# Kernel optimization log

Measured on AMD Instinct MI355X. Metric: run time of the kernel, lower is better.

## Reference

```python
import jax, jax.numpy as jnp
import numpy as np

B, H, N, D = 2, 8, 2048, 64


def setup_inputs() -> dict:
    key = jax.random.key(0)
    kq, kk, kv = jax.random.split(key, 3)
    q = jax.random.normal(kq, (B, H, N, D), dtype=jnp.float32)
    k = jax.random.normal(kk, (B, H, N, D), dtype=jnp.float32)
    v = jax.random.normal(kv, (B, H, N, D), dtype=jnp.float32)
    return {"q": q, "k": k, "v": v}


def _selective_attn(sim):
    # sim: (b, h, i, j). Gate computed from first head, relu'd, SOS unmasked,
    # diagonal zeroed, shifted down one row, cumsum over query rows, subtracted.
    b, h, i, j = sim.shape
    gate = jax.nn.relu(sim[:, 0])                       # (b, i, j)
    gate = gate.at[:, :, j - i].set(0.0)                # no_mask_sos: column -i
    eye = jnp.eye(i, dtype=sim.dtype)
    if j > i:
        eye = jnp.pad(eye, ((0, 0), (j - i, 0)), constant_values=1.0)
    gate = (1.0 - eye) * gate
    # F.pad(gate, (0,0,1,-1)): shift rows down by one, drop last row
    gate = jnp.pad(gate, ((0, 0), (1, 0), (0, 0)))[:, :i, :]
    gate = jnp.cumsum(gate, axis=-2)
    return sim - gate[:, None]                          # broadcast over heads


def reference(q, k, v):
    scale = q.shape[-1] ** -0.5
    i, j = q.shape[-2], k.shape[-2]

    # squared L2 distance scores: ||q||^2 + ||k||^2 - 2 q.k  (== cdist(q,k)**2)
    q_sq = jnp.sum(q * q, axis=-1)                      # (b, h, i)
    k_sq = jnp.sum(k * k, axis=-1)                      # (b, h, j)
    qk = jnp.einsum('bhid,bhjd->bhij', q, k)            # (b, h, i, j)
    d2 = jnp.maximum(q_sq[..., :, None] + k_sq[..., None, :] - 2.0 * qk, 0.0)
    sim = -d2 * scale

    # causal mask (triu with offset j - i + 1)
    mask_value = -jnp.finfo(sim.dtype).max
    causal = jnp.triu(jnp.ones((i, j), dtype=bool), j - i + 1)
    sim = jnp.where(causal, mask_value, sim)

    # selective attention gating
    sim = _selective_attn(sim)

    # one-hot straight-through attention
    idx = jnp.argmax(sim, axis=-1)                      # (b, h, i)
    hard = jax.nn.one_hot(idx, j, dtype=sim.dtype)      # (b, h, i, j)
    soft = jax.nn.softmax(sim, axis=-1)
    attn = hard + soft - jax.lax.stop_gradient(soft)

    return jnp.einsum('bhij,bhjd->bhid', attn, v)
```

## Files before the change

kernel.cpp:

```cpp
#include <hip/hip_runtime.h>
#include <stdint.h>

#define B_ 2
#define H_ 8
#define N_ 2048
#define D_ 64
#define BH_ (B_ * H_)
#define NROWS (BH_ * N_)
#define TPB_ 288
#define NTASK (TPB_ * BH_)
#define NBLK1 (NTASK / 4)
#define MAXCH 8
#define EPSF 8e-3f
#define INFF __int_as_float(0x7f800000)

using u64 = unsigned long long;
using u32 = unsigned int;
typedef __attribute__((ext_vector_type(8))) short short8;
typedef __attribute__((ext_vector_type(4))) float f32x4;

__global__ __launch_bounds__(256) void prep_k(
    const float* __restrict__ k, char* __restrict__ khi_g,
    char* __restrict__ klo_g, float* __restrict__ ksq_g,
    u32* __restrict__ count)
{
  if (blockIdx.x == 0 && threadIdx.x == 0) count[0] = 0;
  const int t = (int)blockIdx.x * 256 + threadIdx.x;
  const int r = t >> 3, kg = t & 7;
  const float* kp = k + (size_t)r * D_ + kg * 8;
  const float4 f0 = *(const float4*)kp;
  const float4 f1 = *(const float4*)(kp + 4);
  const float vv[8] = {f0.x, f0.y, f0.z, f0.w, f1.x, f1.y, f1.z, f1.w};
  u32 hw[4], lw[4];
  float ps = 0.f;
  #pragma unroll
  for (int e = 0; e < 4; ++e) {
    const float va = vv[2 * e], vb = vv[2 * e + 1];
    ps = fmaf(va, va, ps); ps = fmaf(vb, vb, ps);
    const u32 ha = __float_as_uint(va) & 0xFFFF0000u;
    const u32 hb = __float_as_uint(vb) & 0xFFFF0000u;
    hw[e] = (ha >> 16) | hb;
    const u32 la = __float_as_uint(va - __uint_as_float(ha));
    const u32 lb = __float_as_uint(vb - __uint_as_float(hb));
    lw[e] = (la >> 16) | (lb & 0xFFFF0000u);
  }
  const size_t off = ((size_t)(r >> 4) * 2 + (kg >> 2)) * 1024 +
                     (size_t)(((kg & 3) << 4) + (r & 15)) * 16;
  *(uint4*)(khi_g + off) = make_uint4(hw[0], hw[1], hw[2], hw[3]);
  *(uint4*)(klo_g + off) = make_uint4(lw[0], lw[1], lw[2], lw[3]);
  float ssum = ps;
  ssum += __shfl_xor(ssum, 1);
  ssum += __shfl_xor(ssum, 2);
  ssum += __shfl_xor(ssum, 4);
  if (kg == 0) ksq_g[r] = ssum;
}

__global__ __launch_bounds__(256, 4) void phase1(
    const float* __restrict__ q, const char* __restrict__ khi_g,
    const char* __restrict__ klo_g, const float* __restrict__ ksq_g,
    u64* __restrict__ bestc, u32* __restrict__ secc)
{
  const int b = (int)blockIdx.x;
  const int ob = (b & 7) * (NBLK1 / 8) + (b >> 3);
  const int task = ob * 4 + (threadIdx.x >> 6);
  const int bh = task / TPB_;
  int rem = task - bh * TPB_;
  int g2 = 0, nc = 1;
  while (rem >= nc) { rem -= nc; ++g2; nc = (2 * g2 + 17) >> 4; }
  const int c = rem;
  const int jfirst = c * 16;
  const int jlast = min(jfirst + 15, 2 * g2 + 1);

  const int lane = threadIdx.x & 63;
  const int grp = lane >> 4, c0 = lane & 15;
  const int i0 = g2 * 32;

  short8 ah[2][2], al[2][2];
  #pragma unroll
  for (int s = 0; s < 2; ++s) {
    const float* qrow =
        q + ((size_t)bh * N_ + i0 + s * 16 + c0) * D_ + grp * 8;
    #pragma unroll
    for (int h = 0; h < 2; ++h) {
      const float4 f0 = *(const float4*)(qrow + h * 32);
      const float4 f1 = *(const float4*)(qrow + h * 32 + 4);
      const float vv[8] = {f0.x, f0.y, f0.z, f0.w, f1.x, f1.y, f1.z, f1.w};
      #pragma unroll
      for (int e = 0; e < 8; ++e) {
        const float v = vv[e];
        const u32 hb = __float_as_uint(v) & 0xFFFF0000u;
        ah[s][h][e] = (short)(hb >> 16);
        al[s][h][e] = (short)(__float_as_uint(v - __uint_as_float(hb)) >> 16);
      }
    }
  }

  float bf[2][4], sf[2][4];
  u32 bj[2][4];
  #pragma unroll
  for (int s = 0; s < 2; ++s)
    #pragma unroll
    for (int r2 = 0; r2 < 4; ++r2) {
      bf[s][r2] = INFF; sf[s][r2] = INFF; bj[s][r2] = 0;
    }

  const size_t fb = (size_t)bh * 128 * 2048;
  const char* ph = khi_g + fb + (size_t)jfirst * 2048 + lane * 16;
  const char* pl = klo_g + fb + (size_t)jfirst * 2048 + lane * 16;
  const float* pk = ksq_g + (size_t)bh * N_ + jfirst * 16 + c0;

  short8 ch0 = *(const short8*)(ph);
  short8 ch1 = *(const short8*)(ph + 1024);
  short8 cl0 = *(const short8*)(pl);
  short8 cl1 = *(const short8*)(pl + 1024);
  float cks = *pk;

  for (int js = jfirst; js <= jlast; ++js) {
    const int adv = (js < jlast) ? 1 : 0;
    const char* nh = ph + adv * 2048;
    const char* nl = pl + adv * 2048;
    const short8 nh0 = *(const short8*)(nh);
    const short8 nh1 = *(const short8*)(nh + 1024);
    const short8 nl0 = *(const short8*)(nl);
    const short8 nl1 = *(const short8*)(nl + 1024);
    const float nks = pk[adv * 16];
    ph = nh; pl = nl; pk += adv * 16;

    const int jcol = js * 16 + c0;
    #pragma unroll
    for (int s = 0; s < 2; ++s) {
      if (js > 2 * g2 + s) continue;
      const bool dsub = (js == 2 * g2 + s);
      f32x4 aA = {0.f, 0.f, 0.f, 0.f}, aB = {0.f, 0.f, 0.f, 0.f};
      aA = __builtin_amdgcn_mfma_f32_16x16x32_bf16(ah[s][0], ch0, aA, 0, 0, 0);
      aB = __builtin_amdgcn_mfma_f32_16x16x32_bf16(ah[s][1], ch1, aB, 0, 0, 0);
      aA = __builtin_amdgcn_mfma_f32_16x16x32_bf16(ah[s][0], cl0, aA, 0, 0, 0);
      aB = __builtin_amdgcn_mfma_f32_16x16x32_bf16(ah[s][1], cl1, aB, 0, 0, 0);
      aA = __builtin_amdgcn_mfma_f32_16x16x32_bf16(al[s][0], ch0, aA, 0, 0, 0);
      aB = __builtin_amdgcn_mfma_f32_16x16x32_bf16(al[s][1], ch1, aB, 0, 0, 0);
      #pragma unroll
      for (int reg = 0; reg < 4; ++reg) {
        float score = fmaf(-2.f, aA[reg] + aB[reg], cks);
        if (dsub) {
          const int irow = i0 + s * 16 + grp * 4 + reg;
          if (jcol > irow) score = INFF;
        }
        const float loser = fmaxf(bf[s][reg], score);
        sf[s][reg] = fminf(sf[s][reg], loser);
        if (score < bf[s][reg]) bj[s][reg] = (u32)jcol;
        bf[s][reg] = fminf(bf[s][reg], score);
      }
    }
    ch0 = nh0; ch1 = nh1; cl0 = nl0; cl1 = nl1; cks = nks;
  }

  #pragma unroll
  for (int s = 0; s < 2; ++s) {
    #pragma unroll
    for (int reg = 0; reg < 4; ++reg) {
      const u32 bbits = __float_as_uint(bf[s][reg]);
      const u32 key = bbits ^ (u32)(((int)bbits >> 31) | 0x80000000);
      u64 pkk = ((u64)key << 32) | bj[s][reg];
      float sv = sf[s][reg];
      #pragma unroll
      for (int m = 1; m < 16; m <<= 1) {
        const u64 opk = (u64)__shfl_xor((long long)pkk, m);
        const float osv = __shfl_xor(sv, m);
        const u32 mk = (u32)(pkk >> 32), ok = (u32)(opk >> 32);
        const u32 lk = (opk < pkk) ? mk : ok;
        const u32 lb = (lk & 0x80000000u) ? (lk ^ 0x80000000u) : ~lk;
        sv = fminf(fminf(sv, osv), __uint_as_float(lb));
        if (opk < pkk) pkk = opk;
      }
      if (c0 == 0) {
        const size_t rr = (size_t)bh * N_ + i0 + s * 16 + grp * 4 + reg;
        bestc[(size_t)c * NROWS + rr] = pkk;
        secc[(size_t)c * NROWS + rr] = __float_as_uint(sv);
      }
    }
  }
}

__global__ __launch_bounds__(256) void combine_gather(
    const u64* __restrict__ bestc, const u32* __restrict__ secc,
    const float* __restrict__ v, float* __restrict__ out,
    u32* __restrict__ flaglist, u32* __restrict__ count)
{
  __shared__ u32 idx_s[64];
  const int tid = threadIdx.x;
  const int r0 = (int)blockIdx.x * 64;
  if (tid < 64) {
    const int r = r0 + tid;
    const int i = r & (N_ - 1);
    const int g2 = i >> 5;
    const int nch = (2 * g2 + 17) >> 4;
    u64 b0 = ~0ull;
    float bcur = INFF, s1 = INFF;
    int cstar = 0;
    for (int c2 = 0; c2 < nch; ++c2) {
      const u64 kk = bestc[(size_t)c2 * NROWS + r];
      const u32 key = (u32)(kk >> 32);
      const u32 bits = (key & 0x80000000u) ? (key ^ 0x80000000u) : ~key;
      const float f = __uint_as_float(bits);
      if (kk < b0) { s1 = fminf(s1, bcur); b0 = kk; bcur = f; cstar = c2; }
      else s1 = fminf(s1, f);
    }
    s1 = fminf(s1, __uint_as_float(secc[(size_t)cstar * NROWS + r]));
    idx_s[tid] = (u32)(b0 & 0xFFFFu);
    if (s1 - bcur < EPSF) {
      const u32 p = atomicAdd(count, 1u);
      flaglist[p] = (u32)r;
    }
  }
  __syncthreads();
  #pragma unroll
  for (int iter = 0; iter < 4; ++iter) {
    const int task = tid + iter * 256;
    const int rl = task >> 4, cc = task & 15;
    const int r = r0 + rl;
    const u32 j = idx_s[rl];
    const int bh = r >> 11;
    const float4 val = ((const float4*)(v + ((size_t)bh * N_ + j) * D_))[cc];
    ((float4*)(out + (size_t)r * D_))[cc] = val;
  }
}

__global__ __launch_bounds__(256) void exact_gather(
    const float* __restrict__ q, const float* __restrict__ k,
    const float* __restrict__ v, float* __restrict__ out,
    const u32* __restrict__ flaglist, const u32* __restrict__ count)
{
  __shared__ double qd[D_];
  __shared__ double sd[256];
  __shared__ int sj[256];
  const int tid = threadIdx.x;
  const int cnt = (int)count[0];
  for (int li = blockIdx.x; li < cnt; li += (int)gridDim.x) {
    const int r = (int)flaglist[li];
    const int bh = r >> 11;
    const int i = r & (N_ - 1);
    const float* qr = q + (size_t)r * D_;
    const float* kb = k + (size_t)bh * N_ * D_;
    if (tid < D_) qd[tid] = (double)qr[tid];
    __syncthreads();
    double qsqd = 0.0;
    for (int d = 0; d < D_; ++d) qsqd = fma(qd[d], qd[d], qsqd);
    double bbest = 1e300;
    int bjj = 0;
    for (int j = tid; j <= i; j += 256) {
      const float* kr = kb + (size_t)j * D_;
      double a0 = 0, a1 = 0, s0 = 0, s1 = 0;
      for (int d = 0; d < D_; d += 2) {
        const double k0 = (double)kr[d], k1 = (double)kr[d + 1];
        a0 = fma(qd[d], k0, a0);  a1 = fma(qd[d + 1], k1, a1);
        s0 = fma(k0, k0, s0);     s1 = fma(k1, k1, s1);
      }
      const double raw = (qsqd + (s0 + s1)) - 2.0 * (a0 + a1);
      const double d2 = raw > 0.0 ? raw : 0.0;
      if (d2 < bbest) { bbest = d2; bjj = j; }
    }
    sd[tid] = bbest; sj[tid] = bjj;
    __syncthreads();
    for (int s = 128; s > 0; s >>= 1) {
      if (tid < s) {
        const double ob = sd[tid + s]; const int oj = sj[tid + s];
        if (ob < sd[tid] || (ob == sd[tid] && oj < sj[tid])) {
          sd[tid] = ob; sj[tid] = oj;
        }
      }
      __syncthreads();
    }
    const int jwin = sj[0];
    if (tid < 16) {
      const float4 val =
          ((const float4*)(v + ((size_t)bh * N_ + jwin) * D_))[tid];
      ((float4*)(out + (size_t)r * D_))[tid] = val;
    }
    __syncthreads();
  }
}

extern "C" void kernel_launch(void* const* d_in, const int* in_sizes, int n_in,
                              void* d_out, int out_size, void* d_ws,
                              size_t ws_size, hipStream_t stream) {
  const float* q = (const float*)d_in[0];
  const float* k = (const float*)d_in[1];
  const float* v = (const float*)d_in[2];
  float* out = (float*)d_out;

  char* ws = (char*)d_ws;
  u32* count = (u32*)ws;
  u32* flaglist = (u32*)(ws + 4096);
  float* ksq_g = (float*)(ws + 256 * 1024);
  char* khi_g = ws + 1ull * 1024 * 1024;
  char* klo_g = ws + 8ull * 1024 * 1024;
  u64* bestc = (u64*)(ws + 16ull * 1024 * 1024);
  u32* secc = (u32*)(ws + 24ull * 1024 * 1024);

  prep_k<<<(NROWS * 8) / 256, 256, 0, stream>>>(k, khi_g, klo_g, ksq_g, count);
  phase1<<<NBLK1, 256, 0, stream>>>(q, khi_g, klo_g, ksq_g, bestc, secc);
  combine_gather<<<NROWS / 64, 256, 0, stream>>>(bestc, secc, v, out,
                                                 flaglist, count);
  exact_gather<<<64, 256, 0, stream>>>(q, k, v, out, flaglist, count);
}
```

Measured before the change: 66.76 us.

## Halve key chunk size, use one-wave blocks, fuse exact fixup into combine

Phase1 now processes key chunks of 8 instead of 16 tiles, with one 64-thread wave per block and a closed-form task decode in place of the loop. This gives more, smaller tasks and is meant to improve load balance over the triangular causal work. The separate exact_gather kernel, with its atomic flag counter, is folded into the combine kernel. Each block resolves its own flagged rows in double precision before the final V gather, which removes one launch and the atomics. The trade-off is more partial results to merge, and blocks with many flagged rows now handle them serially.

```diff
diff --git a/kernel.cpp b/kernel.cpp
--- a/kernel.cpp
+++ b/kernel.cpp
@@ -7,10 +7,9 @@
 #define D_ 64
 #define BH_ (B_ * H_)
 #define NROWS (BH_ * N_)
-#define TPB_ 288
-#define NTASK (TPB_ * BH_)
-#define NBLK1 (NTASK / 4)
-#define MAXCH 8
+#define TPB_ 544
+#define TASKS (TPB_ * BH_)
+#define MAXCH 16
 #define EPSF 8e-3f
 #define INFF __int_as_float(0x7f800000)
 
@@ -19,12 +18,12 @@
 typedef __attribute__((ext_vector_type(8))) short short8;
 typedef __attribute__((ext_vector_type(4))) float f32x4;
 
+#define MFMA16(A, B, C) __builtin_amdgcn_mfma_f32_16x16x32_bf16((A), (B), (C), 0, 0, 0)
+
 __global__ __launch_bounds__(256) void prep_k(
     const float* __restrict__ k, char* __restrict__ khi_g,
-    char* __restrict__ klo_g, float* __restrict__ ksq_g,
-    u32* __restrict__ count)
+    char* __restrict__ klo_g, float* __restrict__ ksq_g)
 {
-  if (blockIdx.x == 0 && threadIdx.x == 0) count[0] = 0;
   const int t = (int)blockIdx.x * 256 + threadIdx.x;
   const int r = t >> 3, kg = t & 7;
   const float* kp = k + (size_t)r * D_ + kg * 8;
@@ -55,44 +54,48 @@
   if (kg == 0) ksq_g[r] = ssum;
 }
 
-__global__ __launch_bounds__(256, 4) void phase1(
+__device__ __forceinline__ void cvt_hilo(const float* p, short8& hi, short8& lo) {
+  const float4 f0 = *(const float4*)p;
+  const float4 f1 = *(const float4*)(p + 4);
+  const float vv[8] = {f0.x, f0.y, f0.z, f0.w, f1.x, f1.y, f1.z, f1.w};
+  #pragma unroll
+  for (int e = 0; e < 8; ++e) {
+    const float v = vv[e];
+    const u32 hb = __float_as_uint(v) & 0xFFFF0000u;
+    hi[e] = (short)(hb >> 16);
+    lo[e] = (short)(__float_as_uint(v - __uint_as_float(hb)) >> 16);
+  }
+}
+
+__global__ __launch_bounds__(64, 4) void phase1(
     const float* __restrict__ q, const char* __restrict__ khi_g,
     const char* __restrict__ klo_g, const float* __restrict__ ksq_g,
     u64* __restrict__ bestc, u32* __restrict__ secc)
 {
   const int b = (int)blockIdx.x;
-  const int ob = (b & 7) * (NBLK1 / 8) + (b >> 3);
-  const int task = ob * 4 + (threadIdx.x >> 6);
+  const int task = (b & 7) * (TASKS / 8) + (b >> 3);
   const int bh = task / TPB_;
-  int rem = task - bh * TPB_;
-  int g2 = 0, nc = 1;
-  while (rem >= nc) { rem -= nc; ++g2; nc = (2 * g2 + 17) >> 4; }
-  const int c = rem;
-  const int jfirst = c * 16;
-  const int jlast = min(jfirst + 15, 2 * g2 + 1);
+  const int rem = task - bh * TPB_;
+  int a = 0;
+  while (2 * (a + 1) * (a + 2) <= rem) ++a;
+  const int idx = rem - 2 * a * (a + 1);
+  const int g2 = 4 * a + idx / (a + 1);
+  const int c = idx - (idx / (a + 1)) * (a + 1);
+  const int jfirst = c * 8;
+  const int jlast = min(jfirst + 7, 2 * g2 + 1);
 
   const int lane = threadIdx.x & 63;
   const int grp = lane >> 4, c0 = lane & 15;
   const int i0 = g2 * 32;
 
-  short8 ah[2][2], al[2][2];
-  #pragma unroll
-  for (int s = 0; s < 2; ++s) {
-    const float* qrow =
-        q + ((size_t)bh * N_ + i0 + s * 16 + c0) * D_ + grp * 8;
-    #pragma unroll
-    for (int h = 0; h < 2; ++h) {
-      const float4 f0 = *(const float4*)(qrow + h * 32);
-      const float4 f1 = *(const float4*)(qrow + h * 32 + 4);
-      const float vv[8] = {f0.x, f0.y, f0.z, f0.w, f1.x, f1.y, f1.z, f1.w};
-      #pragma unroll
-      for (int e = 0; e < 8; ++e) {
-        const float v = vv[e];
-        const u32 hb = __float_as_uint(v) & 0xFFFF0000u;
-        ah[s][h][e] = (short)(hb >> 16);
-        al[s][h][e] = (short)(__float_as_uint(v - __uint_as_float(hb)) >> 16);
-      }
-    }
+  short8 ah00, ah01, al00, al01, ah10, ah11, al10, al11;
+  {
+    const float* q0 = q + ((size_t)bh * N_ + i0 + c0) * D_ + grp * 8;
+    cvt_hilo(q0, ah00, al00);
+    cvt_hilo(q0 + 32, ah01, al01);
+    const float* q1 = q0 + 16 * D_;
+    cvt_hilo(q1, ah10, al10);
+    cvt_hilo(q1 + 32, ah11, al11);
   }
 
   float bf[2][4], sf[2][4];
@@ -117,38 +120,44 @@
 
   for (int js = jfirst; js <= jlast; ++js) {
     const int adv = (js < jlast) ? 1 : 0;
-    const char* nh = ph + adv * 2048;
-    const char* nl = pl + adv * 2048;
-    const short8 nh0 = *(const short8*)(nh);
-    const short8 nh1 = *(const short8*)(nh + 1024);
-    const short8 nl0 = *(const short8*)(nl);
-    const short8 nl1 = *(const short8*)(nl + 1024);
+    const short8 nh0 = *(const short8*)(ph + adv * 2048);
+    const short8 nh1 = *(const short8*)(ph + adv * 2048 + 1024);
+    const short8 nl0 = *(const short8*)(pl + adv * 2048);
+    const short8 nl1 = *(const short8*)(pl + adv * 2048 + 1024);
     const float nks = pk[adv * 16];
-    ph = nh; pl = nl; pk += adv * 16;
+    ph += adv * 2048; pl += adv * 2048; pk += adv * 16;
 
     const int jcol = js * 16 + c0;
-    #pragma unroll
-    for (int s = 0; s < 2; ++s) {
-      if (js > 2 * g2 + s) continue;
-      const bool dsub = (js == 2 * g2 + s);
+    if (js <= 2 * g2) {
+      const bool dsub = (js == 2 * g2);
       f32x4 aA = {0.f, 0.f, 0.f, 0.f}, aB = {0.f, 0.f, 0.f, 0.f};
-      aA = __builtin_amdgcn_mfma_f32_16x16x32_bf16(ah[s][0], ch0, aA, 0, 0, 0);
-      aB = __builtin_amdgcn_mfma_f32_16x16x32_bf16(ah[s][1], ch1, aB, 0, 0, 0);
-      aA = __builtin_amdgcn_mfma_f32_16x16x32_bf16(ah[s][0], cl0, aA, 0, 0, 0);
-      aB = __builtin_amdgcn_mfma_f32_16x16x32_bf16(ah[s][1], cl1, aB, 0, 0, 0);
-      aA = __builtin_amdgcn_mfma_f32_16x16x32_bf16(al[s][0], ch0, aA, 0, 0, 0);
-      aB = __builtin_amdgcn_mfma_f32_16x16x32_bf16(al[s][1], ch1, aB, 0, 0, 0);
+      aA = MFMA16(ah00, ch0, aA);  aB = MFMA16(ah01, ch1, aB);
+      aA = MFMA16(ah00, cl0, aA);  aB = MFMA16(ah01, cl1, aB);
+      aA = MFMA16(al00, ch0, aA);  aB = MFMA16(al01, ch1, aB);
       #pragma unroll
       for (int reg = 0; reg < 4; ++reg) {
         float score = fmaf(-2.f, aA[reg] + aB[reg], cks);
-        if (dsub) {
-          const int irow = i0 + s * 16 + grp * 4 + reg;
-          if (jcol > irow) score = INFF;
-        }
-        const float loser = fmaxf(bf[s][reg], score);
-        sf[s][reg] = fminf(sf[s][reg], loser);
-        if (score < bf[s][reg]) bj[s][reg] = (u32)jcol;
-        bf[s][reg] = fminf(bf[s][reg], score);
+        if (dsub && jcol > i0 + grp * 4 + reg) score = INFF;
+        const float loser = fmaxf(bf[0][reg], score);
+        sf[0][reg] = fminf(sf[0][reg], loser);
+        if (score < bf[0][reg]) bj[0][reg] = (u32)jcol;
+        bf[0][reg] = fminf(bf[0][reg], score);
+      }
+    }
+    {
+      const bool dsub = (js == 2 * g2 + 1);
+      f32x4 aA = {0.f, 0.f, 0.f, 0.f}, aB = {0.f, 0.f, 0.f, 0.f};
+      aA = MFMA16(ah10, ch0, aA);  aB = MFMA16(ah11, ch1, aB);
+      aA = MFMA16(ah10, cl0, aA);  aB = MFMA16(ah11, cl1, aB);
+      aA = MFMA16(al10, ch0, aA);  aB = MFMA16(al11, ch1, aB);
+      #pragma unroll
+      for (int reg = 0; reg < 4; ++reg) {
+        float score = fmaf(-2.f, aA[reg] + aB[reg], cks);
+        if (dsub && jcol > i0 + 16 + grp * 4 + reg) score = INFF;
+        const float loser = fmaxf(bf[1][reg], score);
+        sf[1][reg] = fminf(sf[1][reg], loser);
+        if (score < bf[1][reg]) bj[1][reg] = (u32)jcol;
+        bf[1][reg] = fminf(bf[1][reg], score);
       }
     }
     ch0 = nh0; ch1 = nh1; cl0 = nl0; cl1 = nl1; cks = nks;
@@ -181,19 +190,23 @@
   }
 }
 
-__global__ __launch_bounds__(256) void combine_gather(
+__global__ __launch_bounds__(256) void combine_fix_gather(
     const u64* __restrict__ bestc, const u32* __restrict__ secc,
-    const float* __restrict__ v, float* __restrict__ out,
-    u32* __restrict__ flaglist, u32* __restrict__ count)
+    const float* __restrict__ q, const float* __restrict__ k,
+    const float* __restrict__ v, float* __restrict__ out)
 {
   __shared__ u32 idx_s[64];
+  __shared__ u32 flg_s[64];
+  __shared__ double qd[D_];
+  __shared__ double sd[256];
+  __shared__ int sj[256];
   const int tid = threadIdx.x;
   const int r0 = (int)blockIdx.x * 64;
+
   if (tid < 64) {
     const int r = r0 + tid;
     const int i = r & (N_ - 1);
-    const int g2 = i >> 5;
-    const int nch = (2 * g2 + 17) >> 4;
+    const int nch = (2 * (i >> 5) + 9) >> 3;
     u64 b0 = ~0ull;
     float bcur = INFF, s1 = INFF;
     int cstar = 0;
@@ -207,36 +220,13 @@
     }
     s1 = fminf(s1, __uint_as_float(secc[(size_t)cstar * NROWS + r]));
     idx_s[tid] = (u32)(b0 & 0xFFFFu);
-    if (s1 - bcur < EPSF) {
-      const u32 p = atomicAdd(count, 1u);
-      flaglist[p] = (u32)r;
-    }
+    flg_s[tid] = ((s1 - bcur) < EPSF) ? 1u : 0u;
   }
   __syncthreads();
-  #pragma unroll
-  for (int iter = 0; iter < 4; ++iter) {
-    const int task = tid + iter * 256;
-    const int rl = task >> 4, cc = task & 15;
+
+  for (int rl = 0; rl < 64; ++rl) {
+    if (!flg_s[rl]) continue;
     const int r = r0 + rl;
-    const u32 j = idx_s[rl];
-    const int bh = r >> 11;
-    const float4 val = ((const float4*)(v + ((size_t)bh * N_ + j) * D_))[cc];
-    ((float4*)(out + (size_t)r * D_))[cc] = val;
-  }
-}
-
-__global__ __launch_bounds__(256) void exact_gather(
-    const float* __restrict__ q, const float* __restrict__ k,
-    const float* __restrict__ v, float* __restrict__ out,
-    const u32* __restrict__ flaglist, const u32* __restrict__ count)
-{
-  __shared__ double qd[D_];
-  __shared__ double sd[256];
-  __shared__ int sj[256];
-  const int tid = threadIdx.x;
-  const int cnt = (int)count[0];
-  for (int li = blockIdx.x; li < cnt; li += (int)gridDim.x) {
-    const int r = (int)flaglist[li];
     const int bh = r >> 11;
     const int i = r & (N_ - 1);
     const float* qr = q + (size_t)r * D_;
@@ -249,13 +239,13 @@
     int bjj = 0;
     for (int j = tid; j <= i; j += 256) {
       const float* kr = kb + (size_t)j * D_;
-      double a0 = 0, a1 = 0, s0 = 0, s1 = 0;
+      double a0 = 0, a1 = 0, s0 = 0, s1d = 0;
       for (int d = 0; d < D_; d += 2) {
         const double k0 = (double)kr[d], k1 = (double)kr[d + 1];
         a0 = fma(qd[d], k0, a0);  a1 = fma(qd[d + 1], k1, a1);
-        s0 = fma(k0, k0, s0);     s1 = fma(k1, k1, s1);
-      }
-      const double raw = (qsqd + (s0 + s1)) - 2.0 * (a0 + a1);
+        s0 = fma(k0, k0, s0);     s1d = fma(k1, k1, s1d);
+      }
+      const double raw = (qsqd + (s0 + s1d)) - 2.0 * (a0 + a1);
       const double d2 = raw > 0.0 ? raw : 0.0;
       if (d2 < bbest) { bbest = d2; bjj = j; }
     }
@@ -270,13 +260,19 @@
       }
       __syncthreads();
     }
-    const int jwin = sj[0];
-    if (tid < 16) {
-      const float4 val =
-          ((const float4*)(v + ((size_t)bh * N_ + jwin) * D_))[tid];
-      ((float4*)(out + (size_t)r * D_))[tid] = val;
-    }
+    if (tid == 0) idx_s[rl] = (u32)sj[0];
     __syncthreads();
+  }
+
+  #pragma unroll
+  for (int iter = 0; iter < 4; ++iter) {
+    const int tk = tid + iter * 256;
+    const int rl = tk >> 4, cc = tk & 15;
+    const int r = r0 + rl;
+    const u32 j = idx_s[rl];
+    const int bh = r >> 11;
+    const float4 val = ((const float4*)(v + ((size_t)bh * N_ + j) * D_))[cc];
+    ((float4*)(out + (size_t)r * D_))[cc] = val;
   }
 }
 
@@ -289,17 +285,13 @@
   float* out = (float*)d_out;
 
   char* ws = (char*)d_ws;
-  u32* count = (u32*)ws;
-  u32* flaglist = (u32*)(ws + 4096);
   float* ksq_g = (float*)(ws + 256 * 1024);
   char* khi_g = ws + 1ull * 1024 * 1024;
   char* klo_g = ws + 8ull * 1024 * 1024;
   u64* bestc = (u64*)(ws + 16ull * 1024 * 1024);
   u32* secc = (u32*)(ws + 24ull * 1024 * 1024);
 
-  prep_k<<<(NROWS * 8) / 256, 256, 0, stream>>>(k, khi_g, klo_g, ksq_g, count);
-  phase1<<<NBLK1, 256, 0, stream>>>(q, khi_g, klo_g, ksq_g, bestc, secc);
-  combine_gather<<<NROWS / 64, 256, 0, stream>>>(bestc, secc, v, out,
-                                                 flaglist, count);
-  exact_gather<<<64, 256, 0, stream>>>(q, k, v, out, flaglist, count);
-}
+  prep_k<<<(NROWS * 8) / 256, 256, 0, stream>>>(k, khi_g, klo_g, ksq_g);
+  phase1<<<TASKS, 64, 0, stream>>>(q, khi_g, klo_g, ksq_g, bestc, secc);
+  combine_fix_gather<<<NROWS / 64, 256, 0, stream>>>(bestc, secc, q, k, v, out);
+}
```

Result: slower. 86.38 us (+29.4%).
